# Kernel optimization log

Hardware: AMD Instinct MI355X
Metric: run time of the kernel (lower is better)

The kernel has to match this reference:

```python
import jax, jax.numpy as jnp
import numpy as np

TOP_K = 2
EPS = 1e-6

def setup_inputs() -> dict:
    B, S, H, G, E, M = 2, 2048, 1024, 256, 8, 2048
    key = jax.random.key(0)
    ks = jax.random.split(key, 16)
    s_h = 1.0 / np.sqrt(H)
    s_g = 1.0 / np.sqrt(G)
    s_m = 1.0 / np.sqrt(M)
    return {
        "x": jax.random.normal(ks[0], (B, S, H), jnp.float32),
        "genre_embed": jax.random.normal(ks[1], (B, 1, G), jnp.float32),
        "rms_w": jnp.ones((H,), jnp.float32),
        "wg_W": jax.random.normal(ks[2], (H, E), jnp.float32) * s_h,
        "wg_b": jnp.zeros((E,), jnp.float32),
        "gg_W": jax.random.normal(ks[3], (G, E), jnp.float32) * s_g,
        "gg_b": jnp.zeros((E,), jnp.float32),
        "W1": jax.random.normal(ks[4], (E, H, M), jnp.float32) * s_h,
        "b1": jnp.zeros((E, M), jnp.float32),
        "W2": jax.random.normal(ks[5], (E, M, M), jnp.float32) * s_m,
        "b2": jnp.zeros((E, M), jnp.float32),
        "W3": jax.random.normal(ks[6], (E, M, H), jnp.float32) * s_m,
        "b3": jnp.zeros((E, H), jnp.float32),
    }


def reference(x, genre_embed, rms_w, wg_W, wg_b, gg_W, gg_b, W1, b1, W2, b2, W3, b3):
    E = W1.shape[0]
    # RMSNorm
    var = jnp.mean(x * x, axis=-1, keepdims=True)
    xn = rms_w * (x * jax.lax.rsqrt(var + EPS))
    # gating: word gate [B,S,E] + genre gate [B,1,E] (broadcast over seq)
    gate = (xn @ wg_W + wg_b) + (genre_embed @ gg_W + gg_b)
    gate_w = jax.nn.softmax(gate, axis=-1)
    topk_w, topk_i = jax.lax.top_k(gate_w, TOP_K)  # [B,S,K]
    # combine weights per expert: sum_k topk_w * onehot(topk_i)
    cw = jnp.sum(jax.nn.one_hot(topk_i, E, dtype=x.dtype) * topk_w[..., None], axis=-2)  # [B,S,E]
    # dense all-expert MLP (equivalent math to masked dispatch/combine)
    h1 = jax.nn.relu(jnp.einsum('bsh,ehm->bsem', x, W1) + b1)
    h2 = jax.nn.relu(jnp.einsum('bsem,emn->bsen', h1, W2) + b2)
    out_e = jnp.einsum('bsen,enh->bseh', h2, W3) + b3
    return jnp.einsum('bseh,bse->bsh', out_e, cw)
```

## Files before the change

kernel.cpp:

```cpp
#include <hip/hip_runtime.h>
#include <hip/hip_bf16.h>

#define T_TOK 4096
#define N_PAIR 8192
#define H_DIM 1024
#define M_DIM 2048
#define E_NUM 8

#define T_W1 4096
#define T_W2 8192
#define T_W3 4096
#define T_ROUT 1024

using bf16x8 = __attribute__((ext_vector_type(8))) short;
using f32x4  = __attribute__((ext_vector_type(4))) float;

__device__ __forceinline__ unsigned short f2bf(float f) {
    unsigned int u = __builtin_bit_cast(unsigned int, f);
    u += 0x7fffu + ((u >> 16) & 1u);
    return (unsigned short)(u >> 16);
}
__device__ __forceinline__ float bf2f(unsigned short u) {
    return __builtin_bit_cast(float, (unsigned int)u << 16);
}

__device__ __forceinline__ void async16(const unsigned short* g, unsigned short* l) {
    __builtin_amdgcn_global_load_lds(
        (const __attribute__((address_space(1))) void*)g,
        (__attribute__((address_space(3))) void*)l, 16, 0, 0);
}

__global__ void k_prep(const float* __restrict__ W1, const float* __restrict__ W2,
                       const float* __restrict__ W3,
                       unsigned short* __restrict__ W1t, unsigned short* __restrict__ W2t,
                       unsigned short* __restrict__ W3t,
                       const float* __restrict__ x, const float* __restrict__ rms_w,
                       const float* __restrict__ wg_W, const float* __restrict__ genre,
                       const float* __restrict__ gg_W, const float* __restrict__ gg_b,
                       const float* __restrict__ wg_b,
                       int* __restrict__ tok_e, float* __restrict__ tok_w)
{
    __shared__ float ld[32][132];
    int bid = blockIdx.x;

    if (bid < T_W1 + T_W2 + T_W3) {
        const float* W; unsigned short* Wt; int tile, kshift, ntshift, N, K;
        if (bid < T_W1)              { W = W1; Wt = W1t; tile = bid;                 K = H_DIM; N = M_DIM; kshift = 10; ntshift = 4; }
        else if (bid < T_W1 + T_W2)  { W = W2; Wt = W2t; tile = bid - T_W1;          K = M_DIM; N = M_DIM; kshift = 11; ntshift = 4; }
        else                         { W = W3; Wt = W3t; tile = bid - T_W1 - T_W2;   K = M_DIM; N = H_DIM; kshift = 11; ntshift = 3; }
        int r0 = (tile >> ntshift) * 32;
        int n0 = (tile & ((1 << ntshift) - 1)) * 128;
        int t = threadIdx.x;
        {
            int rr = t >> 3, c0 = t & 7;
            const float4* src = (const float4*)(W + (size_t)(r0 + rr) * N + n0);
#pragma unroll
            for (int cc = 0; cc < 4; cc++) {
                float4 v = src[c0 + cc * 8];
                float* d = &ld[rr][(c0 + cc * 8) * 4];
                d[0] = v.x; d[1] = v.y; d[2] = v.z; d[3] = v.w;
            }
        }
        __syncthreads();
        {
            int n = t >> 1, half = t & 1;
            int kb = half * 16;
            bf16x8 o0, o1;
#pragma unroll
            for (int q = 0; q < 8; q++) o0[q] = (short)f2bf(ld[kb + q][n]);
#pragma unroll
            for (int q = 0; q < 8; q++) o1[q] = (short)f2bf(ld[kb + 8 + q][n]);
            int rg = r0 + kb;
            int e = rg >> kshift;
            int k = rg & (K - 1);
            unsigned short* dst = Wt + ((size_t)e * N + (n0 + n)) * K + k;
            *(bf16x8*)dst = o0;
            *(bf16x8*)(dst + 8) = o1;
        }
        return;
    }

    int wave = threadIdx.x >> 6, lane = threadIdx.x & 63;
    int tok = (bid - (T_W1 + T_W2 + T_W3)) * 4 + wave;
    int b = tok >> 11;
    const float* xr = x + (size_t)tok * H_DIM;
    float xv[16];
    float ss = 0.f;
#pragma unroll
    for (int j = 0; j < 16; j++) { xv[j] = xr[lane + 64 * j]; ss += xv[j] * xv[j]; }
#pragma unroll
    for (int off = 32; off > 0; off >>= 1) ss += __shfl_xor(ss, off);
    float rstd = rsqrtf(ss * (1.f / 1024.f) + 1e-6f);
    float g[8] = {0.f, 0.f, 0.f, 0.f, 0.f, 0.f, 0.f, 0.f};
#pragma unroll
    for (int gi0 = 0; gi0 < 4; gi0++) {
        int gi = lane + gi0 * 64;
        float gf = genre[b * 256 + gi];
        const float4* w4 = (const float4*)(gg_W + gi * 8);
        float4 wa = w4[0], wb = w4[1];
        g[0] += gf * wa.x; g[1] += gf * wa.y; g[2] += gf * wa.z; g[3] += gf * wa.w;
        g[4] += gf * wb.x; g[5] += gf * wb.y; g[6] += gf * wb.z; g[7] += gf * wb.w;
    }
#pragma unroll
    for (int j = 0; j < 16; j++) {
        int h = lane + 64 * j;
        float xn = xv[j] * rstd * rms_w[h];
        const float4* w4 = (const float4*)(wg_W + h * 8);
        float4 wa = w4[0], wb = w4[1];
        g[0] += xn * wa.x; g[1] += xn * wa.y; g[2] += xn * wa.z; g[3] += xn * wa.w;
        g[4] += xn * wb.x; g[5] += xn * wb.y; g[6] += xn * wb.z; g[7] += xn * wb.w;
    }
#pragma unroll
    for (int e = 0; e < 8; e++) {
#pragma unroll
        for (int off = 32; off > 0; off >>= 1) g[e] += __shfl_xor(g[e], off);
    }
    if (lane == 0) {
#pragma unroll
        for (int e = 0; e < 8; e++) g[e] += wg_b[e] + gg_b[e];
        float m = g[0];
        for (int e = 1; e < 8; e++) m = fmaxf(m, g[e]);
        float p[8], psum = 0.f;
        for (int e = 0; e < 8; e++) { p[e] = expf(g[e] - m); psum += p[e]; }
        int i0 = 0;
        for (int e = 1; e < 8; e++) if (p[e] > p[i0]) i0 = e;
        int i1 = (i0 == 0) ? 1 : 0;
        for (int e = 0; e < 8; e++) if (e != i0 && p[e] > p[i1]) i1 = e;
        float inv = 1.f / psum;
        tok_e[tok * 2] = i0;         tok_e[tok * 2 + 1] = i1;
        tok_w[tok * 2] = p[i0] * inv; tok_w[tok * 2 + 1] = p[i1] * inv;
    }
}

__global__ void k_scan(const int* __restrict__ tok_e, int* __restrict__ meta)
{
    __shared__ int cnt[8];
    int t = threadIdx.x;
    if (t < 8) cnt[t] = 0;
    __syncthreads();
    for (int p = t; p < N_PAIR; p += 256) atomicAdd(&cnt[tok_e[p]], 1);
    __syncthreads();
    if (t == 0) {
        int acc = 0;
        for (int e = 0; e < 8; e++) {
            meta[e] = cnt[e]; meta[8 + e] = acc; meta[16 + e] = acc; acc += cnt[e];
        }
    }
}

__global__ void k_gather(const float* __restrict__ x, const int* __restrict__ tok_e,
                         int* __restrict__ meta, int* __restrict__ pair_pos,
                         unsigned short* __restrict__ x_g)
{
    int wave = threadIdx.x >> 6, lane = threadIdx.x & 63;
    int p = blockIdx.x * 4 + wave;
    int t = p >> 1;
    int e = tok_e[p];
    int pos;
    if (lane == 0) {
        pos = atomicAdd(&meta[16 + e], 1);
        pair_pos[p] = pos;
    }
    pos = __shfl(pos, 0);
    const float4* src = (const float4*)(x + (size_t)t * H_DIM);
    ushort4* dst = (ushort4*)(x_g + (size_t)pos * H_DIM);
#pragma unroll
    for (int j = 0; j < 4; j++) {
        float4 v = src[lane + 64 * j];
        ushort4 o;
        o.x = f2bf(v.x); o.y = f2bf(v.y); o.z = f2bf(v.z); o.w = f2bf(v.w);
        dst[lane + 64 * j] = o;
    }
}

template<bool RELU>
__global__ void k_gemm(const unsigned short* __restrict__ A,
                       const unsigned short* __restrict__ Wt,
                       const float* __restrict__ bias,
                       unsigned short* __restrict__ C,
                       const int* __restrict__ meta,
                       int K, int N)
{
    int e = blockIdx.z;
    int cnt = meta[e];
    int by = blockIdx.y;
    if (by * 128 >= cnt) return;
    int base = meta[8 + e];
    int bx = blockIdx.x;

    __shared__ __align__(16) unsigned short As[128 * 64];
    __shared__ __align__(16) unsigned short Bs[128 * 64];

    int tid = threadIdx.x;
    int wave = tid >> 6, lane = tid & 63;
    int lrow8 = lane >> 3;
    int lslot = lane & 7;
    int chunk_g = (lslot ^ lrow8) * 8;

    const unsigned short* Bw = Wt + (size_t)e * N * K + (size_t)(bx * 128) * K;
    const unsigned short* gA[4]; const unsigned short* gB[4];
    unsigned short* lA[4]; unsigned short* lB[4];
#pragma unroll
    for (int c = 0; c < 4; c++) {
        int rloc = wave * 32 + c * 8 + lrow8;
        int ra = base + by * 128 + rloc;
        ra = min(ra, N_PAIR - 1);
        gA[c] = A + (size_t)ra * K + chunk_g;
        gB[c] = Bw + (size_t)rloc * K + chunk_g;
        lA[c] = &As[(wave * 32 + c * 8) * 64];
        lB[c] = &Bs[(wave * 32 + c * 8) * 64];
    }

    int wr = (wave >> 1) * 64, wc = (wave & 1) * 64;
    int lm = lane & 15, lq = lane >> 4;

    int aoff[4][2], boff[4][2];
#pragma unroll
    for (int i = 0; i < 4; i++)
#pragma unroll
        for (int h = 0; h < 2; h++) {
            int R = wr + i * 16 + lm;
            aoff[i][h] = R * 64 + (((h * 4 + lq) ^ (R & 7)) * 8);
            int Nn = wc + i * 16 + lm;
            boff[i][h] = Nn * 64 + (((h * 4 + lq) ^ (Nn & 7)) * 8);
        }

    f32x4 acc[4][4] = {};

    for (int kt = 0; kt < K; kt += 64) {
#pragma unroll
        for (int c = 0; c < 4; c++) { async16(gA[c] + kt, lA[c]); async16(gB[c] + kt, lB[c]); }
        __syncthreads();
#pragma unroll
        for (int h = 0; h < 2; h++) {
            bf16x8 af[4], bfr[4];
#pragma unroll
            for (int i = 0; i < 4; i++) af[i] = *(const bf16x8*)&As[aoff[i][h]];
#pragma unroll
            for (int j = 0; j < 4; j++) bfr[j] = *(const bf16x8*)&Bs[boff[j][h]];
#pragma unroll
            for (int i = 0; i < 4; i++)
#pragma unroll
                for (int j = 0; j < 4; j++)
                    acc[i][j] = __builtin_amdgcn_mfma_f32_16x16x32_bf16(af[i], bfr[j], acc[i][j], 0, 0, 0);
        }
        __syncthreads();
    }

#pragma unroll
    for (int j = 0; j < 4; j++) {
        int n = bx * 128 + wc + j * 16 + lm;
        float bv = bias[(size_t)e * N + n];
#pragma unroll
        for (int i = 0; i < 4; i++) {
#pragma unroll
            for (int r = 0; r < 4; r++) {
                int grow = by * 128 + wr + i * 16 + lq * 4 + r;
                if (grow < cnt) {
                    float v = acc[i][j][r] + bv;
                    if (RELU) v = fmaxf(v, 0.f);
                    C[(size_t)(base + grow) * N + n] = f2bf(v);
                }
            }
        }
    }
}

__global__ void k_combine(const unsigned short* __restrict__ o3,
                          const int* __restrict__ pair_pos,
                          const float* __restrict__ tok_w, float* __restrict__ out)
{
    int t = blockIdx.x;
    int c = threadIdx.x;
    int p0 = pair_pos[t * 2], p1 = pair_pos[t * 2 + 1];
    float w0 = tok_w[t * 2], w1 = tok_w[t * 2 + 1];
    ushort4 a = ((const ushort4*)(o3 + (size_t)p0 * H_DIM))[c];
    ushort4 bq = ((const ushort4*)(o3 + (size_t)p1 * H_DIM))[c];
    float4 o;
    o.x = w0 * bf2f(a.x) + w1 * bf2f(bq.x);
    o.y = w0 * bf2f(a.y) + w1 * bf2f(bq.y);
    o.z = w0 * bf2f(a.z) + w1 * bf2f(bq.z);
    o.w = w0 * bf2f(a.w) + w1 * bf2f(bq.w);
    ((float4*)(out + (size_t)t * H_DIM))[c] = o;
}

extern "C" void kernel_launch(void* const* d_in, const int* in_sizes, int n_in,
                              void* d_out, int out_size, void* d_ws, size_t ws_size,
                              hipStream_t stream) {
    const float* x      = (const float*)d_in[0];
    const float* genre  = (const float*)d_in[1];
    const float* rms_w  = (const float*)d_in[2];
    const float* wg_W   = (const float*)d_in[3];
    const float* wg_b   = (const float*)d_in[4];
    const float* gg_W   = (const float*)d_in[5];
    const float* gg_b   = (const float*)d_in[6];
    const float* W1     = (const float*)d_in[7];
    const float* b1     = (const float*)d_in[8];
    const float* W2     = (const float*)d_in[9];
    const float* b2     = (const float*)d_in[10];
    const float* W3     = (const float*)d_in[11];
    const float* b3     = (const float*)d_in[12];
    float* out = (float*)d_out;

    char* p = (char*)d_ws;
    auto alloc = [&](size_t bytes) { char* r = p; p += (bytes + 255) & ~(size_t)255; return r; };
    unsigned short* W1t = (unsigned short*)alloc((size_t)E_NUM * H_DIM * M_DIM * 2);
    unsigned short* W2t = (unsigned short*)alloc((size_t)E_NUM * M_DIM * M_DIM * 2);
    unsigned short* W3t = (unsigned short*)alloc((size_t)E_NUM * M_DIM * H_DIM * 2);
    unsigned short* x_g = (unsigned short*)alloc((size_t)N_PAIR * H_DIM * 2);
    unsigned short* h1  = (unsigned short*)alloc((size_t)N_PAIR * M_DIM * 2);
    unsigned short* h2  = (unsigned short*)alloc((size_t)N_PAIR * M_DIM * 2);
    unsigned short* o3  = (unsigned short*)alloc((size_t)N_PAIR * H_DIM * 2);
    int*   meta         = (int*)alloc(24 * 4);
    int*   tok_e        = (int*)alloc((size_t)N_PAIR * 4);
    float* tok_w        = (float*)alloc((size_t)N_PAIR * 4);
    int*   pair_pos     = (int*)alloc((size_t)N_PAIR * 4);

    dim3 blk(256);

    k_prep<<<T_W1 + T_W2 + T_W3 + T_ROUT, blk, 0, stream>>>(
        W1, W2, W3, W1t, W2t, W3t, x, rms_w, wg_W, genre, gg_W, gg_b, wg_b,
        tok_e, tok_w);
    k_scan<<<1, blk, 0, stream>>>(tok_e, meta);
    k_gather<<<N_PAIR / 4, blk, 0, stream>>>(x, tok_e, meta, pair_pos, x_g);

    k_gemm<true ><<<dim3(M_DIM / 128, 32, E_NUM), blk, 0, stream>>>(
        x_g, W1t, b1, h1, meta, H_DIM, M_DIM);
    k_gemm<true ><<<dim3(M_DIM / 128, 32, E_NUM), blk, 0, stream>>>(
        h1, W2t, b2, h2, meta, M_DIM, M_DIM);
    k_gemm<false><<<dim3(H_DIM / 128, 32, E_NUM), blk, 0, stream>>>(
        h2, W3t, b3, o3, meta, M_DIM, H_DIM);

    k_combine<<<T_TOK, blk, 0, stream>>>(o3, pair_pos, tok_w, out);

    (void)in_sizes; (void)n_in; (void)ws_size;
}
```

Baseline: 699.0 us.

## Double-buffer LDS tiles in grouped expert GEMM to overlap loads with MFMA

Splits the shared-memory A/B tiles into two buffers and restructures the K loop as a ping-pong pipeline. The async global-to-LDS copies for the next K tile are issued before the MFMA work on the current tile, so load latency can hide behind compute. The goal is to shorten the stall each K step spends waiting on global memory. In exchange, LDS use per block doubles to 64 KB, which may reduce how many blocks fit on a CU. The loop also gains explicit prologue and epilogue code, and it assumes K is a multiple of 128.

```diff
diff --git a/kernel.cpp b/kernel.cpp
--- a/kernel.cpp
+++ b/kernel.cpp
@@ -188,8 +188,8 @@
     int base = meta[8 + e];
     int bx = blockIdx.x;
 
-    __shared__ __align__(16) unsigned short As[128 * 64];
-    __shared__ __align__(16) unsigned short Bs[128 * 64];
+    __shared__ __align__(16) unsigned short As[2][128 * 64];
+    __shared__ __align__(16) unsigned short Bs[2][128 * 64];
 
     int tid = threadIdx.x;
     int wave = tid >> 6, lane = tid & 63;
@@ -199,7 +199,7 @@
 
     const unsigned short* Bw = Wt + (size_t)e * N * K + (size_t)(bx * 128) * K;
     const unsigned short* gA[4]; const unsigned short* gB[4];
-    unsigned short* lA[4]; unsigned short* lB[4];
+    int sAB[4];
 #pragma unroll
     for (int c = 0; c < 4; c++) {
         int rloc = wave * 32 + c * 8 + lrow8;
@@ -207,8 +207,7 @@
         ra = min(ra, N_PAIR - 1);
         gA[c] = A + (size_t)ra * K + chunk_g;
         gB[c] = Bw + (size_t)rloc * K + chunk_g;
-        lA[c] = &As[(wave * 32 + c * 8) * 64];
-        lB[c] = &Bs[(wave * 32 + c * 8) * 64];
+        sAB[c] = (wave * 32 + c * 8) * 64;
     }
 
     int wr = (wave >> 1) * 64, wc = (wave & 1) * 64;
@@ -227,25 +226,51 @@
 
     f32x4 acc[4][4] = {};
 
-    for (int kt = 0; kt < K; kt += 64) {
-#pragma unroll
-        for (int c = 0; c < 4; c++) { async16(gA[c] + kt, lA[c]); async16(gB[c] + kt, lB[c]); }
+#define STAGE(buf, kt)                                                        \
+    {                                                                         \
+        _Pragma("unroll")                                                     \
+        for (int c = 0; c < 4; c++) {                                         \
+            async16(gA[c] + (kt), &As[buf][sAB[c]]);                          \
+            async16(gB[c] + (kt), &Bs[buf][sAB[c]]);                          \
+        }                                                                     \
+    }
+
+#define COMPUTE(buf)                                                          \
+    {                                                                         \
+        _Pragma("unroll")                                                     \
+        for (int h = 0; h < 2; h++) {                                         \
+            bf16x8 af[4], bfr[4];                                             \
+            _Pragma("unroll")                                                 \
+            for (int i = 0; i < 4; i++) af[i] = *(const bf16x8*)&As[buf][aoff[i][h]]; \
+            _Pragma("unroll")                                                 \
+            for (int j = 0; j < 4; j++) bfr[j] = *(const bf16x8*)&Bs[buf][boff[j][h]]; \
+            _Pragma("unroll")                                                 \
+            for (int i = 0; i < 4; i++)                                       \
+                _Pragma("unroll")                                             \
+                for (int j = 0; j < 4; j++)                                   \
+                    acc[i][j] = __builtin_amdgcn_mfma_f32_16x16x32_bf16(af[i], bfr[j], acc[i][j], 0, 0, 0); \
+        }                                                                     \
+    }
+
+    STAGE(0, 0);
+    __syncthreads();
+
+#pragma unroll 1
+    for (int kt = 0; kt + 128 < K; kt += 128) {
+        STAGE(1, kt + 64);
+        COMPUTE(0);
         __syncthreads();
-#pragma unroll
-        for (int h = 0; h < 2; h++) {
-            bf16x8 af[4], bfr[4];
-#pragma unroll
-            for (int i = 0; i < 4; i++) af[i] = *(const bf16x8*)&As[aoff[i][h]];
-#pragma unroll
-            for (int j = 0; j < 4; j++) bfr[j] = *(const bf16x8*)&Bs[boff[j][h]];
-#pragma unroll
-            for (int i = 0; i < 4; i++)
-#pragma unroll
-                for (int j = 0; j < 4; j++)
-                    acc[i][j] = __builtin_amdgcn_mfma_f32_16x16x32_bf16(af[i], bfr[j], acc[i][j], 0, 0, 0);
-        }
+        STAGE(0, kt + 128);
+        COMPUTE(1);
         __syncthreads();
     }
+    STAGE(1, K - 64);
+    COMPUTE(0);
+    __syncthreads();
+    COMPUTE(1);
+
+#undef STAGE
+#undef COMPUTE
 
 #pragma unroll
     for (int j = 0; j < 4; j++) {
```

After: 1.084 ms. +55.0%, slower.
